# Optimization experiments

Hardware: AMD Instinct MI355X
Metric: run time of the kernel (lower is better)

## Reference

```python
import jax, jax.numpy as jnp
import numpy as np

NA = 3        # num anchors
NM = 32       # num prototype masks
NC = 80       # num classes
STRIDE = 8    # network stride
THRESH = 0.05 # conf threshold


def setup_inputs() -> dict:
    key = jax.random.key(0)
    nB, nH, nW = 16, 80, 80
    channels = NA * (5 + NC) + NA * NM  # 351
    output = jax.random.normal(key, (nB, channels, nH, nW), dtype=jnp.float32)
    # anchors already in output-grid units (pixel anchors / stride), shape [NA, 2] = (w, h)
    anchors = jnp.array([[1.25, 1.625], [2.0, 3.75], [4.125, 2.875]], dtype=jnp.float32)
    return {"output": output, "anchors": anchors}


def reference(output, anchors):
    nB, channels, nH, nW = output.shape
    nHW = nH * nW
    # split box head and mask-coefficient head
    box = output[:, :NA * (5 + NC)].reshape(nB, NA, 5 + NC, nHW)
    mask_out = output[:, NA * (5 + NC):].reshape(nB, NA, NM, nHW).transpose(0, 1, 3, 2)  # [nB,NA,nHW,NM]

    lin_y, lin_x = jnp.meshgrid(jnp.arange(nH, dtype=output.dtype),
                                jnp.arange(nW, dtype=output.dtype), indexing='ij')
    lin_x = lin_x.reshape(-1)
    lin_y = lin_y.reshape(-1)

    anchor_wh = anchors.reshape(1, NA, 2, 1)  # broadcast over [nB,NA,2,nHW]
    max_value = jnp.floor(jnp.log(jnp.asarray(1e35, output.dtype) / anchors.max() / STRIDE))

    xs = jax.nn.sigmoid(box[:, :, 0]) + lin_x                                   # [nB,NA,nHW]
    ys = jax.nn.sigmoid(box[:, :, 1]) + lin_y                                   # [nB,NA,nHW]
    wh = jnp.exp(jnp.minimum(box[:, :, 2:4], max_value)) * anchor_wh            # [nB,NA,2,nHW]
    obj = jax.nn.sigmoid(box[:, :, 4])                                          # [nB,NA,nHW]

    cls = jax.nn.softmax(box[:, :, 5:], axis=2)                                 # [nB,NA,NC,nHW]
    cls_max = cls.max(axis=2)
    cls_idx = cls.argmax(axis=2).astype(output.dtype)
    score = cls_max * obj                                                        # [nB,NA,nHW]

    keep = score > THRESH
    b, a, p = jnp.nonzero(keep)  # eager: data-dependent detection count N

    coords = jnp.stack([xs[b, a, p], ys[b, a, p], wh[b, a, 0, p], wh[b, a, 1, p]], axis=1) * STRIDE  # [N,4]
    mc = mask_out[b, a, p]                                                        # [N,NM]
    return jnp.concatenate([
        b[:, None].astype(output.dtype),
        coords,
        mc,
        score[b, a, p][:, None],
        cls_idx[b, a, p][:, None],
    ], axis=1)  # [N, 7+NM]
```

## Files before the change

### kernel.cpp

```cpp
#include <hip/hip_runtime.h>
#include <math.h>

#define NA 3
#define NM 32
#define NC 80
#define STRIDE_PX 8.0f
#define THRESH 0.05f
#define NB 16
#define NH 80
#define NW 80
#define NHW (NH * NW)
#define CH (NA * (5 + NC) + NA * NM)
#define BOXCH (NA * (5 + NC))
#define TOTAL (NB * NA * NHW)
#define BLK 256
#define NBLK (TOTAL / BLK)
#define ROWSZ 39
#define ROWPAD 40
#define WS_ROW_STRIDE (BLK * ROWPAD)

__device__ __forceinline__ int wave_sum64(int v) {
#pragma unroll
  for (int s = 32; s > 0; s >>= 1) v += __shfl_xor(v, s, 64);
  return v;
}

__global__ __launch_bounds__(BLK, 6) void decode_kernel(
    const float* __restrict__ in, const float* __restrict__ anchors,
    float* __restrict__ wsrows, int* __restrict__ counts) {
  int g = blockIdx.x * BLK + threadIdx.x;
  int p = g % NHW;
  int a = (g / NHW) % NA;
  int b = g / (NA * NHW);

  const float* base = in + ((size_t)b * CH + (size_t)a * (5 + NC)) * NHW + p;

  float tx = base[0];
  float ty = base[(size_t)1 * NHW];
  float tw = base[(size_t)2 * NHW];
  float th = base[(size_t)3 * NHW];
  float tobj = base[(size_t)4 * NHW];

  float m = -INFINITY, s = 0.f;
  int idx = 0;
#pragma unroll
  for (int c = 0; c < NC; c += 16) {
    float x[16];
#pragma unroll
    for (int j = 0; j < 16; ++j) x[j] = base[(size_t)(5 + c + j) * NHW];

    float m8[8]; int i8[8];
#pragma unroll
    for (int k = 0; k < 8; ++k) {
      bool gt = x[2 * k + 1] > x[2 * k];
      m8[k] = gt ? x[2 * k + 1] : x[2 * k];
      i8[k] = gt ? (2 * k + 1) : (2 * k);
    }
    float m4[4]; int i4[4];
#pragma unroll
    for (int k = 0; k < 4; ++k) {
      bool gt = m8[2 * k + 1] > m8[2 * k];
      m4[k] = gt ? m8[2 * k + 1] : m8[2 * k];
      i4[k] = gt ? i8[2 * k + 1] : i8[2 * k];
    }
    float m2[2]; int i2[2];
#pragma unroll
    for (int k = 0; k < 2; ++k) {
      bool gt = m4[2 * k + 1] > m4[2 * k];
      m2[k] = gt ? m4[2 * k + 1] : m4[2 * k];
      i2[k] = gt ? i4[2 * k + 1] : i4[2 * k];
    }
    bool gtc = m2[1] > m2[0];
    float mc = gtc ? m2[1] : m2[0];
    int ic = (gtc ? i2[1] : i2[0]) + c;

    float e[16];
#pragma unroll
    for (int j = 0; j < 16; ++j) e[j] = __expf(x[j] - mc);
    float s8[8];
#pragma unroll
    for (int k = 0; k < 8; ++k) s8[k] = e[2 * k] + e[2 * k + 1];
    float s4[4];
#pragma unroll
    for (int k = 0; k < 4; ++k) s4[k] = s8[2 * k] + s8[2 * k + 1];
    float sc = (s4[0] + s4[1]) + (s4[2] + s4[3]);

    float mn = fmaxf(m, mc);
    s = s * __expf(m - mn) + sc * __expf(mc - mn);
    idx = (mc > m) ? ic : idx;
    m = mn;
  }

  float cls_max = 1.0f / s;
  float obj = 1.0f / (1.0f + __expf(-tobj));
  float score = cls_max * obj;

  float amax = fmaxf(fmaxf(fmaxf(anchors[0], anchors[1]), fmaxf(anchors[2], anchors[3])),
                     fmaxf(anchors[4], anchors[5]));
  float max_value = floorf(logf(1e35f / amax / STRIDE_PX));
  float aw = anchors[a * 2 + 0];
  float ah = anchors[a * 2 + 1];

  float xs = 1.0f / (1.0f + __expf(-tx)) + (float)(p % NW);
  float ys = 1.0f / (1.0f + __expf(-ty)) + (float)(p / NW);
  float w = __expf(fminf(tw, max_value)) * aw;
  float h = __expf(fminf(th, max_value)) * ah;

  bool keep = score > THRESH;
  unsigned long long ball = __ballot(keep);
  int lane = threadIdx.x & 63;
  int wv = threadIdx.x >> 6;
  int lower = __popcll(ball & ((1ull << lane) - 1ull));
  __shared__ int wc[BLK / 64];
  if (lane == 0) wc[wv] = __popcll(ball);
  __syncthreads();
  int pre = 0;
#pragma unroll
  for (int i = 0; i < BLK / 64; ++i)
    if (i < wv) pre += wc[i];

  if (keep) {
    int lrank = pre + lower;
    float4* o4 = reinterpret_cast<float4*>(
        wsrows + (size_t)blockIdx.x * WS_ROW_STRIDE + (size_t)lrank * ROWPAD);
    const float* mbase = in + ((size_t)b * CH + BOXCH + (size_t)a * NM) * NHW + p;

    float4 v;
    v.x = (float)b; v.y = xs * STRIDE_PX; v.z = ys * STRIDE_PX; v.w = w * STRIDE_PX;
    o4[0] = v;
    v.x = h * STRIDE_PX; v.y = mbase[0]; v.z = mbase[(size_t)1 * NHW]; v.w = mbase[(size_t)2 * NHW];
    o4[1] = v;
#pragma unroll
    for (int gq = 2; gq <= 8; ++gq) {
      v.x = mbase[(size_t)(4 * gq - 5) * NHW];
      v.y = mbase[(size_t)(4 * gq - 4) * NHW];
      v.z = mbase[(size_t)(4 * gq - 3) * NHW];
      v.w = mbase[(size_t)(4 * gq - 2) * NHW];
      o4[gq] = v;
    }
    v.x = mbase[(size_t)31 * NHW]; v.y = score; v.z = (float)idx; v.w = 0.f;
    o4[9] = v;
  }
  if (threadIdx.x == 0)
    counts[blockIdx.x] = wc[0] + wc[1] + wc[2] + wc[3];
}

__global__ __launch_bounds__(BLK, 8) void emit_kernel(
    const float* __restrict__ wsrows, const int* __restrict__ counts,
    float* __restrict__ out, int out_size) {
  int bid = blockIdx.x;
  int t = threadIdx.x;

  int partial = 0;
  for (int j = t; j < bid; j += BLK) partial += counts[j];
  partial = wave_sum64(partial);
  __shared__ int sh[BLK / 64];
  if ((t & 63) == 0) sh[t >> 6] = partial;
  __syncthreads();
  int off = sh[0] + sh[1] + sh[2] + sh[3];

  int cnt = counts[bid];
  int nelem = cnt * ROWSZ;
  const float* src = wsrows + (size_t)bid * WS_ROW_STRIDE;
  int dbase = off * ROWSZ;
  for (int e = t; e < nelem; e += BLK) {
    int row = (int)(((unsigned)e * 107547u) >> 22);
    int col = e - row * 39;
    int d = dbase + e;
    if (d < out_size) out[d] = src[row * ROWPAD + col];
  }
}

extern "C" void kernel_launch(void* const* d_in, const int* in_sizes, int n_in,
                              void* d_out, int out_size, void* d_ws, size_t ws_size,
                              hipStream_t stream) {
  const float* in = (const float*)d_in[0];
  const float* anchors = (const float*)d_in[1];

  float* wsrows = (float*)d_ws;
  int* counts = (int*)((float*)d_ws + (size_t)NBLK * WS_ROW_STRIDE);

  decode_kernel<<<NBLK, BLK, 0, stream>>>(in, anchors, wsrows, counts);
  emit_kernel<<<NBLK, BLK, 0, stream>>>(wsrows, counts, (float*)d_out, out_size);
}
```

Measured before the change: 226.4 us.

## Move mask-coefficient gather into emit kernel with compact per-detection headers

Result: slower. 261.6 us (+15.6%).

```diff
diff --git a/kernel.cpp b/kernel.cpp
--- a/kernel.cpp
+++ b/kernel.cpp
@@ -16,8 +16,7 @@
 #define BLK 256
 #define NBLK (TOTAL / BLK)
 #define ROWSZ 39
-#define ROWPAD 40
-#define WS_ROW_STRIDE (BLK * ROWPAD)
+#define HDR 8
 
 __device__ __forceinline__ int wave_sum64(int v) {
 #pragma unroll
@@ -25,9 +24,9 @@
   return v;
 }
 
-__global__ __launch_bounds__(BLK, 6) void decode_kernel(
+__global__ __launch_bounds__(BLK, 4) void decode_kernel(
     const float* __restrict__ in, const float* __restrict__ anchors,
-    float* __restrict__ wsrows, int* __restrict__ counts) {
+    float* __restrict__ wshdr, int* __restrict__ counts) {
   int g = blockIdx.x * BLK + threadIdx.x;
   int p = g % NHW;
   int a = (g / NHW) % NA;
@@ -44,24 +43,17 @@
   float m = -INFINITY, s = 0.f;
   int idx = 0;
 #pragma unroll
-  for (int c = 0; c < NC; c += 16) {
-    float x[16];
+  for (int c = 0; c < NC; c += 8) {
+    float x[8];
 #pragma unroll
-    for (int j = 0; j < 16; ++j) x[j] = base[(size_t)(5 + c + j) * NHW];
+    for (int j = 0; j < 8; ++j) x[j] = base[(size_t)(5 + c + j) * NHW];
 
-    float m8[8]; int i8[8];
-#pragma unroll
-    for (int k = 0; k < 8; ++k) {
-      bool gt = x[2 * k + 1] > x[2 * k];
-      m8[k] = gt ? x[2 * k + 1] : x[2 * k];
-      i8[k] = gt ? (2 * k + 1) : (2 * k);
-    }
     float m4[4]; int i4[4];
 #pragma unroll
     for (int k = 0; k < 4; ++k) {
-      bool gt = m8[2 * k + 1] > m8[2 * k];
-      m4[k] = gt ? m8[2 * k + 1] : m8[2 * k];
-      i4[k] = gt ? i8[2 * k + 1] : i8[2 * k];
+      bool gt = x[2 * k + 1] > x[2 * k];
+      m4[k] = gt ? x[2 * k + 1] : x[2 * k];
+      i4[k] = gt ? (2 * k + 1) : (2 * k);
     }
     float m2[2]; int i2[2];
 #pragma unroll
@@ -74,16 +66,11 @@
     float mc = gtc ? m2[1] : m2[0];
     int ic = (gtc ? i2[1] : i2[0]) + c;
 
-    float e[16];
-#pragma unroll
-    for (int j = 0; j < 16; ++j) e[j] = __expf(x[j] - mc);
-    float s8[8];
-#pragma unroll
-    for (int k = 0; k < 8; ++k) s8[k] = e[2 * k] + e[2 * k + 1];
-    float s4[4];
-#pragma unroll
-    for (int k = 0; k < 4; ++k) s4[k] = s8[2 * k] + s8[2 * k + 1];
-    float sc = (s4[0] + s4[1]) + (s4[2] + s4[3]);
+    float e0 = __expf(x[0] - mc), e1 = __expf(x[1] - mc);
+    float e2 = __expf(x[2] - mc), e3 = __expf(x[3] - mc);
+    float e4 = __expf(x[4] - mc), e5 = __expf(x[5] - mc);
+    float e6 = __expf(x[6] - mc), e7 = __expf(x[7] - mc);
+    float sc = ((e0 + e1) + (e2 + e3)) + ((e4 + e5) + (e6 + e7));
 
     float mn = fmaxf(m, mc);
     s = s * __expf(m - mn) + sc * __expf(mc - mn);
@@ -91,9 +78,7 @@
     m = mn;
   }
 
-  float cls_max = 1.0f / s;
-  float obj = 1.0f / (1.0f + __expf(-tobj));
-  float score = cls_max * obj;
+  float score = (1.0f / s) * (1.0f / (1.0f + __expf(-tobj)));
 
   float amax = fmaxf(fmaxf(fmaxf(anchors[0], anchors[1]), fmaxf(anchors[2], anchors[3])),
                      fmaxf(anchors[4], anchors[5]));
@@ -122,32 +107,20 @@
   if (keep) {
     int lrank = pre + lower;
     float4* o4 = reinterpret_cast<float4*>(
-        wsrows + (size_t)blockIdx.x * WS_ROW_STRIDE + (size_t)lrank * ROWPAD);
-    const float* mbase = in + ((size_t)b * CH + BOXCH + (size_t)a * NM) * NHW + p;
-
+        wshdr + ((size_t)blockIdx.x * BLK + (size_t)lrank) * HDR);
     float4 v;
     v.x = (float)b; v.y = xs * STRIDE_PX; v.z = ys * STRIDE_PX; v.w = w * STRIDE_PX;
     o4[0] = v;
-    v.x = h * STRIDE_PX; v.y = mbase[0]; v.z = mbase[(size_t)1 * NHW]; v.w = mbase[(size_t)2 * NHW];
+    v.x = h * STRIDE_PX; v.y = score; v.z = (float)idx; v.w = __int_as_float(g);
     o4[1] = v;
-#pragma unroll
-    for (int gq = 2; gq <= 8; ++gq) {
-      v.x = mbase[(size_t)(4 * gq - 5) * NHW];
-      v.y = mbase[(size_t)(4 * gq - 4) * NHW];
-      v.z = mbase[(size_t)(4 * gq - 3) * NHW];
-      v.w = mbase[(size_t)(4 * gq - 2) * NHW];
-      o4[gq] = v;
-    }
-    v.x = mbase[(size_t)31 * NHW]; v.y = score; v.z = (float)idx; v.w = 0.f;
-    o4[9] = v;
   }
   if (threadIdx.x == 0)
     counts[blockIdx.x] = wc[0] + wc[1] + wc[2] + wc[3];
 }
 
-__global__ __launch_bounds__(BLK, 8) void emit_kernel(
-    const float* __restrict__ wsrows, const int* __restrict__ counts,
-    float* __restrict__ out, int out_size) {
+__global__ __launch_bounds__(BLK, 4) void emit_kernel(
+    const float* __restrict__ in, const float* __restrict__ wshdr,
+    const int* __restrict__ counts, float* __restrict__ out, int out_size) {
   int bid = blockIdx.x;
   int t = threadIdx.x;
 
@@ -160,15 +133,37 @@
   int off = sh[0] + sh[1] + sh[2] + sh[3];
 
   int cnt = counts[bid];
-  int nelem = cnt * ROWSZ;
-  const float* src = wsrows + (size_t)bid * WS_ROW_STRIDE;
-  int dbase = off * ROWSZ;
-  for (int e = t; e < nelem; e += BLK) {
-    int row = (int)(((unsigned)e * 107547u) >> 22);
-    int col = e - row * 39;
-    int d = dbase + e;
-    if (d < out_size) out[d] = src[row * ROWPAD + col];
-  }
+  if (t >= cnt) return;
+
+  const float4* h4 = reinterpret_cast<const float4*>(
+      wshdr + ((size_t)bid * BLK + (size_t)t) * HDR);
+  float4 h0 = h4[0];
+  float4 h1 = h4[1];
+  int g = __float_as_int(h1.w);
+  int p = g % NHW;
+  int a = (g / NHW) % NA;
+  int b = g / (NA * NHW);
+
+  int dbase = (off + t) * ROWSZ;
+#define ST(o, v)                       \
+  do {                                 \
+    int dd = dbase + (o);              \
+    if (dd < out_size) out[dd] = (v);  \
+  } while (0)
+
+  ST(0, h0.x);
+  ST(1, h0.y);
+  ST(2, h0.z);
+  ST(3, h0.w);
+  ST(4, h1.x);
+
+  const float* mbase = in + ((size_t)b * CH + BOXCH + (size_t)a * NM) * NHW + p;
+#pragma unroll
+  for (int mm = 0; mm < NM; ++mm) ST(5 + mm, mbase[(size_t)mm * NHW]);
+
+  ST(5 + NM, h1.y);
+  ST(6 + NM, h1.z);
+#undef ST
 }
 
 extern "C" void kernel_launch(void* const* d_in, const int* in_sizes, int n_in,
@@ -177,9 +172,9 @@
   const float* in = (const float*)d_in[0];
   const float* anchors = (const float*)d_in[1];
 
-  float* wsrows = (float*)d_ws;
-  int* counts = (int*)((float*)d_ws + (size_t)NBLK * WS_ROW_STRIDE);
+  float* wshdr = (float*)d_ws;
+  int* counts = (int*)((float*)d_ws + (size_t)NBLK * BLK * HDR);
 
-  decode_kernel<<<NBLK, BLK, 0, stream>>>(in, anchors, wsrows, counts);
-  emit_kernel<<<NBLK, BLK, 0, stream>>>(wsrows, counts, (float*)d_out, out_size);
+  decode_kernel<<<NBLK, BLK, 0, stream>>>(in, anchors, wshdr, counts);
+  emit_kernel<<<NBLK, BLK, 0, stream>>>(in, wshdr, counts, (float*)d_out, out_size);
 }
```
